# Kernel tuning notes

Hardware: AMD Instinct MI355X
Metric: run time of the kernel (lower is better)

The kernel has to match this reference:

```python
import jax, jax.numpy as jnp
import numpy as np

B, S, D = 4, 2048, 1024
H = 16
HD = D // H  # 64


def setup_inputs() -> dict:
    key = jax.random.key(0)
    ks = jax.random.split(key, 5)
    s = 0.02
    return {
        "x": jax.random.normal(ks[0], (B, S, D), dtype=jnp.float32),
        "w_qkv": jax.random.normal(ks[1], (D, 3 * D), dtype=jnp.float32) * s,
        "b_qkv": jnp.zeros((3 * D,), dtype=jnp.float32),
        "w_out": jax.random.normal(ks[2], (D, D), dtype=jnp.float32) * s,
        "b_out": jnp.zeros((D,), dtype=jnp.float32),
    }


def reference(x, w_qkv, b_qkv, w_out, b_out):
    b, s, d = x.shape
    qkv = x @ w_qkv + b_qkv                              # [b,s,3d]
    qkv = qkv.reshape(b, s, 3, H, HD)
    q = qkv[:, :, 0].transpose(0, 2, 1, 3)               # [b,h,s,hd]
    k = qkv[:, :, 1].transpose(0, 2, 1, 3)
    v = qkv[:, :, 2].transpose(0, 2, 1, 3)
    scale = 1.0 / jnp.sqrt(jnp.asarray(HD, dtype=x.dtype))
    scores = jnp.einsum("bhqd,bhkd->bhqk", q, k) * scale  # [b,h,s,s]
    causal = jnp.tril(jnp.ones((s, s), dtype=bool))
    scores = jnp.where(causal[None, None], scores, jnp.asarray(-jnp.inf, dtype=x.dtype))
    probs = jax.nn.softmax(scores, axis=-1)
    out = jnp.einsum("bhqk,bhkd->bhqd", probs, v)        # [b,h,s,hd]
    out = out.transpose(0, 2, 1, 3).reshape(b, s, d)
    return out @ w_out + b_out
```

## Files before the change

kernel.cpp:

```cpp
#include <hip/hip_runtime.h>
#include <hip/hip_bf16.h>

typedef __bf16 bf16_t;
typedef __bf16 bf16x4 __attribute__((ext_vector_type(4)));
typedef __bf16 bf16x8 __attribute__((ext_vector_type(8)));
typedef float f32x4 __attribute__((ext_vector_type(4)));

#define Bb 4
#define Ss 2048
#define Dd 1024
#define Hh 16
#define HDd 64

#define QSC 0.1803368801111244f

__device__ __forceinline__ void gld16(const bf16_t* g, bf16_t* l) {
  __builtin_amdgcn_global_load_lds(
      (const __attribute__((address_space(1))) unsigned int*)g,
      (__attribute__((address_space(3))) unsigned int*)l, 16, 0, 0);
}

__global__ __launch_bounds__(256) void prep(
    const float* __restrict__ x, bf16_t* __restrict__ Xc,
    const float* __restrict__ w_qkv, bf16_t* __restrict__ Wt1) {
  __shared__ bf16_t tile[32][33];
  const int b = blockIdx.x;
  const int tid = threadIdx.x;
  if (b < 8192) {
    int i = (b * 256 + tid) * 4;
    float4 v = *(const float4*)&x[i];
    bf16x4 o = {(bf16_t)v.x, (bf16_t)v.y, (bf16_t)v.z, (bf16_t)v.w};
    *(bf16x4*)&Xc[i] = o;
  } else {
    const int id = b - 8192;
    const int c0 = (id % 96) * 32, r0 = (id / 96) * 32;
    const int tx = tid & 31, ty = tid >> 5;
#pragma unroll
    for (int j = 0; j < 32; j += 8)
      tile[ty + j][tx] = (bf16_t)w_qkv[(size_t)(r0 + ty + j) * 3072 + c0 + tx];
    __syncthreads();
#pragma unroll
    for (int j = 0; j < 32; j += 8)
      Wt1[(size_t)(c0 + ty + j) * 1024 + r0 + tx] = tile[tx][ty + j];
  }
}

__global__ __launch_bounds__(256) void transpose_conv(
    const float* __restrict__ in, bf16_t* __restrict__ out, int R, int C) {
  __shared__ bf16_t tile[32][33];
  int c0 = blockIdx.x * 32, r0 = blockIdx.y * 32;
  int tx = threadIdx.x, ty = threadIdx.y;
#pragma unroll
  for (int j = 0; j < 32; j += 8)
    tile[ty + j][tx] = (bf16_t)in[(size_t)(r0 + ty + j) * C + c0 + tx];
  __syncthreads();
#pragma unroll
  for (int j = 0; j < 32; j += 8)
    out[(size_t)(c0 + ty + j) * R + r0 + tx] = tile[tx][ty + j];
}

template <int MODE>
__global__ __launch_bounds__(512, 2) void gemm_8p(
    const bf16_t* __restrict__ A, const bf16_t* __restrict__ Bt,
    const float* __restrict__ bias, float* __restrict__ outf,
    bf16_t* __restrict__ out0, bf16_t* __restrict__ out1,
    bf16_t* __restrict__ out2, int M, int N, int K) {
  const int tid = threadIdx.x;
  const int lane = tid & 63;
  const int wave = tid >> 6;
  const int quad = lane >> 4;
  const int lr = lane & 15;
  const int wr = wave >> 1;
  const int wc = wave & 1;
  const int m0 = blockIdx.y * 256;
  const int n0 = blockIdx.x * 128;

  __shared__ __align__(16) bf16_t As[3][256 * 64];
  __shared__ __align__(16) bf16_t Bs[3][128 * 64];

  const f32x4 zero = {0.f, 0.f, 0.f, 0.f};
  f32x4 acc[4][4];
#pragma unroll
  for (int mi = 0; mi < 4; ++mi)
#pragma unroll
    for (int ni = 0; ni < 4; ++ni) acc[mi][ni] = zero;

  int ar[4], ac[4], br[2], bc[2];
#pragma unroll
  for (int i = 0; i < 4; ++i) {
    int c = tid + i * 512;
    ar[i] = c >> 3;
    ac[i] = ((c & 7) ^ (ar[i] & 7)) * 8;
  }
#pragma unroll
  for (int i = 0; i < 2; ++i) {
    int c = tid + i * 512;
    br[i] = c >> 3;
    bc[i] = ((c & 7) ^ (br[i] & 7)) * 8;
  }

  const int nk = K >> 6;

  auto stageA = [&](int t, int s) {
    const int ko = t << 6;
#pragma unroll
    for (int i = 0; i < 4; ++i)
      gld16(&A[(size_t)(m0 + ar[i]) * K + ko + ac[i]],
            &As[s][(tid + i * 512) * 8]);
  };
  auto stageB = [&](int t, int s) {
    const int ko = t << 6;
#pragma unroll
    for (int i = 0; i < 2; ++i)
      gld16(&Bt[(size_t)(n0 + br[i]) * K + ko + bc[i]],
            &Bs[s][(tid + i * 512) * 8]);
  };

  stageA(0, 0); stageB(0, 0);
  stageA(1, 1); stageB(1, 1);
  asm volatile("s_waitcnt vmcnt(6)" ::: "memory");
  __builtin_amdgcn_s_barrier();

  const int sx = lr & 7;
  const int arow = wr * 64 + lr;
  const int brow = wc * 64 + lr;

  int scur = 0;
  for (int t = 0; t < nk; ++t) {
    const bf16_t* as = As[scur];
    const bf16_t* bs = Bs[scur];
    int s2 = scur + 2;
    if (s2 >= 3) s2 -= 3;
    const bool pre = (t + 2 < nk);
#pragma unroll
    for (int ks = 0; ks < 2; ++ks) {
      bf16x8 af[4], bfr[4];
      const int cx = (((ks << 2) | quad) ^ sx) * 8;
#pragma unroll
      for (int mi = 0; mi < 4; ++mi)
        af[mi] = *(const bf16x8*)&as[(arow + mi * 16) * 64 + cx];
#pragma unroll
      for (int ni = 0; ni < 4; ++ni)
        bfr[ni] = *(const bf16x8*)&bs[(brow + ni * 16) * 64 + cx];
      if (ks == 0) {
        if (pre) stageA(t + 2, s2);
      } else {
        if (pre) stageB(t + 2, s2);
      }
      __builtin_amdgcn_s_barrier();
      asm volatile("s_waitcnt lgkmcnt(0)" ::: "memory");
      __builtin_amdgcn_sched_barrier(0);
      __builtin_amdgcn_s_setprio(1);
#pragma unroll
      for (int mi = 0; mi < 4; ++mi)
#pragma unroll
        for (int ni = 0; ni < 4; ++ni)
          acc[mi][ni] = __builtin_amdgcn_mfma_f32_16x16x32_bf16(
              af[mi], bfr[ni], acc[mi][ni], 0, 0, 0);
      __builtin_amdgcn_s_setprio(0);
      if (ks == 0) {
        __builtin_amdgcn_s_barrier();
      } else if (t + 1 < nk) {
        if (pre)
          asm volatile("s_waitcnt vmcnt(6)" ::: "memory");
        else
          asm volatile("s_waitcnt vmcnt(0)" ::: "memory");
        __builtin_amdgcn_s_barrier();
      }
    }
    scur = (scur == 2) ? 0 : scur + 1;
  }

#pragma unroll
  for (int mi = 0; mi < 4; ++mi) {
    const int mbase = m0 + wr * 64 + mi * 16 + quad * 4;
#pragma unroll
    for (int ni = 0; ni < 4; ++ni) {
      const int n = n0 + wc * 64 + ni * 16 + lr;
      const float bv = bias[n];
      if (MODE == 1) {
#pragma unroll
        for (int r = 0; r < 4; ++r)
          outf[(size_t)(mbase + r) * N + n] = acc[mi][ni][r] + bv;
      } else {
        const int which = n >> 10;
        const int h = (n >> 6) & 15;
        const int hd = n & 63;
        const int b = mbase >> 11;
        const int s = mbase & 2047;
        if (which == 2) {
          bf16x4 pk = {(bf16_t)(acc[mi][ni][0] + bv),
                       (bf16_t)(acc[mi][ni][1] + bv),
                       (bf16_t)(acc[mi][ni][2] + bv),
                       (bf16_t)(acc[mi][ni][3] + bv)};
          *(bf16x4*)&out2[(((size_t)(b * Hh + h)) * HDd + hd) * Ss + s] = pk;
        } else {
          bf16_t* dst = (which == 0) ? out0 : out1;
          const float sc = (which == 0) ? QSC : 1.0f;
#pragma unroll
          for (int r = 0; r < 4; ++r)
            dst[(((size_t)(b * Hh + h)) * Ss + s + r) * HDd + hd] =
                (bf16_t)((acc[mi][ni][r] + bv) * sc);
        }
      }
    }
  }
}

__global__ __launch_bounds__(256) void attn_kernel(
    const bf16_t* __restrict__ Qg, const bf16_t* __restrict__ Kg,
    const bf16_t* __restrict__ Vtg, bf16_t* __restrict__ Og) {
  const int tid = threadIdx.x;
  const int lane = tid & 63;
  const int wave = tid >> 6;
  const int quad = lane >> 4;
  const int lr = lane & 15;
  const int l7 = lr & 7;

  const int bid = blockIdx.x;
  const int xcd = bid & 7;
  const int j = bid >> 3;
  const int bh = xcd * 8 + (j >> 3);
  const int p = j & 7;
  const int b = bh >> 4;
  const int h = bh & 15;
  const int wq = wave * 32;

  const bf16_t* Qp = Qg + (size_t)bh * Ss * HDd;
  const bf16_t* Kp = Kg + (size_t)bh * Ss * HDd;
  const bf16_t* Vp = Vtg + (size_t)bh * HDd * Ss;

  __shared__ bf16_t Ks[2][64 * 64];
  __shared__ bf16_t Vts[2][64 * 64];
  __shared__ bf16_t Ps[4][32 * 64];

  bf16x8 kreg[2], vreg[2];
  const int r0 = tid >> 3;
  const int c0 = (tid & 7) * 8;
  const int swz = ((tid & 7) ^ ((tid >> 3) & 7)) * 8;

  const f32x4 zero = {0.f, 0.f, 0.f, 0.f};
  bf16x8 ones1;
#pragma unroll
  for (int i = 0; i < 8; ++i) ones1[i] = (bf16_t)1.0f;

#pragma unroll
  for (int i = 0; i < 2; ++i) {
    kreg[i] = *(const bf16x8*)&Kp[(size_t)(r0 + i * 32) * HDd + c0];
    vreg[i] = *(const bf16x8*)&Vp[(size_t)(r0 + i * 32) * Ss + c0];
  }

  int cur = 0;
  for (int half = 0; half < 2; ++half) {
    const int qt = half ? p : 15 - p;
    const int qbase = qt * 128;
    const int ktiles = qt * 2 + 2;

    bf16x8 bq[2][2];
#pragma unroll
    for (int qt2 = 0; qt2 < 2; ++qt2)
#pragma unroll
      for (int kk2 = 0; kk2 < 2; ++kk2)
        bq[qt2][kk2] = *(const bf16x8*)&Qp[(size_t)(qbase + wq + qt2 * 16 +
                                                    lr) *
                                               HDd +
                                           kk2 * 32 + quad * 8];

    f32x4 oacc[4][2];
#pragma unroll
    for (int dt = 0; dt < 4; ++dt)
#pragma unroll
      for (int qt2 = 0; qt2 < 2; ++qt2) oacc[dt][qt2] = zero;
    f32x4 lacc[2];
    lacc[0] = zero;
    lacc[1] = zero;

    for (int kt = 0; kt < ktiles; ++kt) {
      const int kbase = kt * 64;

#pragma unroll
      for (int i = 0; i < 2; ++i) {
        *(bf16x8*)&Ks[cur][(r0 + i * 32) * 64 + swz] = kreg[i];
        *(bf16x8*)&Vts[cur][(r0 + i * 32) * 64 + swz] = vreg[i];
      }
      __syncthreads();

      const int nkb = (kt + 1 < ktiles) ? kbase + 64 : 0;
#pragma unroll
      for (int i = 0; i < 2; ++i) {
        kreg[i] = *(const bf16x8*)&Kp[(size_t)(nkb + r0 + i * 32) * HDd + c0];
        vreg[i] = *(const bf16x8*)&Vp[(size_t)(r0 + i * 32) * Ss + nkb + c0];
      }

      f32x4 sacc[4][2];
#pragma unroll
      for (int kt4 = 0; kt4 < 4; ++kt4)
#pragma unroll
        for (int qt2 = 0; qt2 < 2; ++qt2) sacc[kt4][qt2] = zero;
#pragma unroll
      for (int kk2 = 0; kk2 < 2; ++kk2) {
        const int rsl = (((kk2 << 2) | quad) ^ l7) * 8;
        bf16x8 ak[4];
#pragma unroll
        for (int kt4 = 0; kt4 < 4; ++kt4)
          ak[kt4] = *(const bf16x8*)&Ks[cur][(kt4 * 16 + lr) * 64 + rsl];
#pragma unroll
        for (int kt4 = 0; kt4 < 4; ++kt4)
#pragma unroll
          for (int qt2 = 0; qt2 < 2; ++qt2)
            sacc[kt4][qt2] = __builtin_amdgcn_mfma_f32_16x16x32_bf16(
                ak[kt4], bq[qt2][kk2], sacc[kt4][qt2], 0, 0, 0);
      }

      const bool edge = (kt >= 2 * qt);
#pragma unroll
      for (int kt4 = 0; kt4 < 4; ++kt4)
#pragma unroll
        for (int qt2 = 0; qt2 < 2; ++qt2)
#pragma unroll
          for (int r = 0; r < 4; ++r) {
            float s = sacc[kt4][qt2][r];
            if (edge) {
              const int qg = qbase + wq + qt2 * 16 + lr;
              const int kg = kbase + kt4 * 16 + quad * 4 + r;
              if (kg > qg) s = -1e30f;
            }
            sacc[kt4][qt2][r] = __builtin_amdgcn_exp2f(s);
          }

#pragma unroll
      for (int kt4 = 0; kt4 < 4; ++kt4) {
        const int psl = ((kt4 * 2 + (quad >> 1)) ^ l7) * 8 + (quad & 1) * 4;
#pragma unroll
        for (int qt2 = 0; qt2 < 2; ++qt2) {
          bf16x4 pk = {(bf16_t)sacc[kt4][qt2][0], (bf16_t)sacc[kt4][qt2][1],
                       (bf16_t)sacc[kt4][qt2][2], (bf16_t)sacc[kt4][qt2][3]};
          *(bf16x4*)&Ps[wave][(qt2 * 16 + lr) * 64 + psl] = pk;
        }
      }

#pragma unroll
      for (int kk2 = 0; kk2 < 2; ++kk2) {
        const int rsl = (((kk2 << 2) | quad) ^ l7) * 8;
        bf16x8 av[4], bp[2];
#pragma unroll
        for (int dt = 0; dt < 4; ++dt)
          av[dt] = *(const bf16x8*)&Vts[cur][(dt * 16 + lr) * 64 + rsl];
#pragma unroll
        for (int qt2 = 0; qt2 < 2; ++qt2)
          bp[qt2] = *(const bf16x8*)&Ps[wave][(qt2 * 16 + lr) * 64 + rsl];
#pragma unroll
        for (int dt = 0; dt < 4; ++dt)
#pragma unroll
          for (int qt2 = 0; qt2 < 2; ++qt2)
            oacc[dt][qt2] = __builtin_amdgcn_mfma_f32_16x16x32_bf16(
                av[dt], bp[qt2], oacc[dt][qt2], 0, 0, 0);
#pragma unroll
        for (int qt2 = 0; qt2 < 2; ++qt2)
          lacc[qt2] = __builtin_amdgcn_mfma_f32_16x16x32_bf16(
              ones1, bp[qt2], lacc[qt2], 0, 0, 0);
      }
      cur ^= 1;
    }

#pragma unroll
    for (int qt2 = 0; qt2 < 2; ++qt2) {
      const float inv = 1.f / lacc[qt2][0];
      const int qg = qbase + wq + qt2 * 16 + lr;
#pragma unroll
      for (int dt = 0; dt < 4; ++dt) {
        bf16x4 ov = {(bf16_t)(oacc[dt][qt2][0] * inv),
                     (bf16_t)(oacc[dt][qt2][1] * inv),
                     (bf16_t)(oacc[dt][qt2][2] * inv),
                     (bf16_t)(oacc[dt][qt2][3] * inv)};
        *(bf16x4*)&Og[((size_t)b * Ss + qg) * Dd + h * HDd + dt * 16 +
                      quad * 4] = ov;
      }
    }
  }
}

extern "C" void kernel_launch(void* const* d_in, const int* in_sizes, int n_in,
                              void* d_out, int out_size, void* d_ws,
                              size_t ws_size, hipStream_t stream) {
  const float* x = (const float*)d_in[0];
  const float* w_qkv = (const float*)d_in[1];
  const float* b_qkv = (const float*)d_in[2];
  const float* w_out = (const float*)d_in[3];
  const float* b_out = (const float*)d_in[4];
  float* out = (float*)d_out;

  bf16_t* Kb = (bf16_t*)d_ws;
  bf16_t* Vt = Kb + (size_t)Bb * Hh * Ss * HDd;
  bf16_t* slot3 = Vt + (size_t)Bb * Hh * Ss * HDd;
  bf16_t* Wt1 = slot3;
  bf16_t* Ob = slot3;
  bf16_t* Wt2 = Kb;
  bf16_t* Qb = (bf16_t*)d_out;
  bf16_t* Xc = (bf16_t*)d_out + (size_t)8192 * 1024;

  prep<<<11264, 256, 0, stream>>>(x, Xc, w_qkv, Wt1);

  gemm_8p<0><<<dim3(24, 32), 512, 0, stream>>>(
      Xc, Wt1, b_qkv, nullptr, Qb, Kb, Vt, 8192, 3072, 1024);

  attn_kernel<<<dim3(512), 256, 0, stream>>>(Qb, Kb, Vt, Ob);

  transpose_conv<<<dim3(32, 32), dim3(32, 8), 0, stream>>>(w_out, Wt2, 1024,
                                                           1024);

  gemm_8p<1><<<dim3(8, 32), 512, 0, stream>>>(
      Ob, Wt2, b_out, out, nullptr, nullptr, nullptr, 8192, 1024, 1024);
}
```

Before: 263.4 us.

## Use 256x256 tile GEMM for QKV projection and scalar row-sum in attention

Adds a gemm_wide kernel that computes the QKV projection with 256x256 output tiles, a K-step of 32 and a 4-stage LDS ring. Each wave now holds an 8x4 accumulator block, which raises arithmetic intensity and halves the number of blocks. In attention, the softmax denominator is no longer computed with extra MFMAs against a ones vector. Instead each lane accumulates its exp values in a float and a cross-lane shuffle reduction finishes the sum. The larger tile doubles accumulator register pressure with the 2-block occupancy hint, and the fp32 sum is taken before rounding to bf16, so it differs slightly from the bf16 P actually used in P·V.

```diff
diff --git a/kernel.cpp b/kernel.cpp
--- a/kernel.cpp
+++ b/kernel.cpp
@@ -60,7 +60,7 @@
 }
 
 template <int MODE>
-__global__ __launch_bounds__(512, 2) void gemm_8p(
+__global__ __launch_bounds__(512, 2) void gemm_wide(
     const bf16_t* __restrict__ A, const bf16_t* __restrict__ Bt,
     const float* __restrict__ bias, float* __restrict__ outf,
     bf16_t* __restrict__ out0, bf16_t* __restrict__ out1,
@@ -70,110 +70,107 @@
   const int wave = tid >> 6;
   const int quad = lane >> 4;
   const int lr = lane & 15;
-  const int wr = wave >> 1;
-  const int wc = wave & 1;
+  const int wr = wave >> 2;
+  const int wc = wave & 3;
   const int m0 = blockIdx.y * 256;
-  const int n0 = blockIdx.x * 128;
-
-  __shared__ __align__(16) bf16_t As[3][256 * 64];
-  __shared__ __align__(16) bf16_t Bs[3][128 * 64];
+  const int n0 = blockIdx.x * 256;
+
+  __shared__ __align__(16) bf16_t As[4][256 * 32];
+  __shared__ __align__(16) bf16_t Bs[4][256 * 32];
 
   const f32x4 zero = {0.f, 0.f, 0.f, 0.f};
-  f32x4 acc[4][4];
-#pragma unroll
-  for (int mi = 0; mi < 4; ++mi)
+  f32x4 acc[8][4];
+#pragma unroll
+  for (int mi = 0; mi < 8; ++mi)
 #pragma unroll
     for (int ni = 0; ni < 4; ++ni) acc[mi][ni] = zero;
 
-  int ar[4], ac[4], br[2], bc[2];
-#pragma unroll
-  for (int i = 0; i < 4; ++i) {
-    int c = tid + i * 512;
-    ar[i] = c >> 3;
-    ac[i] = ((c & 7) ^ (ar[i] & 7)) * 8;
-  }
+  int sr[2], sc[2];
 #pragma unroll
   for (int i = 0; i < 2; ++i) {
     int c = tid + i * 512;
-    br[i] = c >> 3;
-    bc[i] = ((c & 7) ^ (br[i] & 7)) * 8;
-  }
-
-  const int nk = K >> 6;
+    sr[i] = c >> 2;
+    sc[i] = ((c & 3) ^ ((sr[i] >> 1) & 3)) * 8;
+  }
+
+  const int nk = K >> 5;
 
   auto stageA = [&](int t, int s) {
-    const int ko = t << 6;
-#pragma unroll
-    for (int i = 0; i < 4; ++i)
-      gld16(&A[(size_t)(m0 + ar[i]) * K + ko + ac[i]],
+    const int ko = t << 5;
+#pragma unroll
+    for (int i = 0; i < 2; ++i)
+      gld16(&A[(size_t)(m0 + sr[i]) * K + ko + sc[i]],
             &As[s][(tid + i * 512) * 8]);
   };
   auto stageB = [&](int t, int s) {
-    const int ko = t << 6;
+    const int ko = t << 5;
 #pragma unroll
     for (int i = 0; i < 2; ++i)
-      gld16(&Bt[(size_t)(n0 + br[i]) * K + ko + bc[i]],
+      gld16(&Bt[(size_t)(n0 + sr[i]) * K + ko + sc[i]],
             &Bs[s][(tid + i * 512) * 8]);
   };
 
   stageA(0, 0); stageB(0, 0);
   stageA(1, 1); stageB(1, 1);
-  asm volatile("s_waitcnt vmcnt(6)" ::: "memory");
+  asm volatile("s_waitcnt vmcnt(4)" ::: "memory");
   __builtin_amdgcn_s_barrier();
 
-  const int sx = lr & 7;
-  const int arow = wr * 64 + lr;
-  const int brow = wc * 64 + lr;
-
-  int scur = 0;
+  const int cx = (quad ^ ((lr >> 1) & 3)) * 8;
+  const int abase = wr * 128 + lr;
+  const int bbase = wc * 64 + lr;
+
   for (int t = 0; t < nk; ++t) {
-    const bf16_t* as = As[scur];
-    const bf16_t* bs = Bs[scur];
-    int s2 = scur + 2;
-    if (s2 >= 3) s2 -= 3;
+    const bf16_t* as = As[t & 3];
+    const bf16_t* bs = Bs[t & 3];
+    const int s2 = (t + 2) & 3;
     const bool pre = (t + 2 < nk);
-#pragma unroll
-    for (int ks = 0; ks < 2; ++ks) {
-      bf16x8 af[4], bfr[4];
-      const int cx = (((ks << 2) | quad) ^ sx) * 8;
-#pragma unroll
-      for (int mi = 0; mi < 4; ++mi)
-        af[mi] = *(const bf16x8*)&as[(arow + mi * 16) * 64 + cx];
+    bf16x8 af[4], bfr[4];
+#pragma unroll
+    for (int ni = 0; ni < 4; ++ni)
+      bfr[ni] = *(const bf16x8*)&bs[(bbase + ni * 16) * 32 + cx];
+#pragma unroll
+    for (int mi = 0; mi < 4; ++mi)
+      af[mi] = *(const bf16x8*)&as[(abase + mi * 16) * 32 + cx];
+    if (pre) stageA(t + 2, s2);
+    __builtin_amdgcn_s_barrier();
+    asm volatile("s_waitcnt lgkmcnt(0)" ::: "memory");
+    __builtin_amdgcn_sched_barrier(0);
+    __builtin_amdgcn_s_setprio(1);
+#pragma unroll
+    for (int mi = 0; mi < 4; ++mi)
 #pragma unroll
       for (int ni = 0; ni < 4; ++ni)
-        bfr[ni] = *(const bf16x8*)&bs[(brow + ni * 16) * 64 + cx];
-      if (ks == 0) {
-        if (pre) stageA(t + 2, s2);
-      } else {
-        if (pre) stageB(t + 2, s2);
-      }
+        acc[mi][ni] = __builtin_amdgcn_mfma_f32_16x16x32_bf16(
+            af[mi], bfr[ni], acc[mi][ni], 0, 0, 0);
+    __builtin_amdgcn_s_setprio(0);
+    __builtin_amdgcn_s_barrier();
+#pragma unroll
+    for (int mi = 0; mi < 4; ++mi)
+      af[mi] = *(const bf16x8*)&as[(abase + (mi + 4) * 16) * 32 + cx];
+    if (pre) stageB(t + 2, s2);
+    __builtin_amdgcn_s_barrier();
+    asm volatile("s_waitcnt lgkmcnt(0)" ::: "memory");
+    __builtin_amdgcn_sched_barrier(0);
+    __builtin_amdgcn_s_setprio(1);
+#pragma unroll
+    for (int mi = 0; mi < 4; ++mi)
+#pragma unroll
+      for (int ni = 0; ni < 4; ++ni)
+        acc[mi + 4][ni] = __builtin_amdgcn_mfma_f32_16x16x32_bf16(
+            af[mi], bfr[ni], acc[mi + 4][ni], 0, 0, 0);
+    __builtin_amdgcn_s_setprio(0);
+    if (t + 1 < nk) {
+      if (pre)
+        asm volatile("s_waitcnt vmcnt(4)" ::: "memory");
+      else
+        asm volatile("s_waitcnt vmcnt(0)" ::: "memory");
       __builtin_amdgcn_s_barrier();
-      asm volatile("s_waitcnt lgkmcnt(0)" ::: "memory");
-      __builtin_amdgcn_sched_barrier(0);
-      __builtin_amdgcn_s_setprio(1);
-#pragma unroll
-      for (int mi = 0; mi < 4; ++mi)
-#pragma unroll
-        for (int ni = 0; ni < 4; ++ni)
-          acc[mi][ni] = __builtin_amdgcn_mfma_f32_16x16x32_bf16(
-              af[mi], bfr[ni], acc[mi][ni], 0, 0, 0);
-      __builtin_amdgcn_s_setprio(0);
-      if (ks == 0) {
-        __builtin_amdgcn_s_barrier();
-      } else if (t + 1 < nk) {
-        if (pre)
-          asm volatile("s_waitcnt vmcnt(6)" ::: "memory");
-        else
-          asm volatile("s_waitcnt vmcnt(0)" ::: "memory");
-        __builtin_amdgcn_s_barrier();
-      }
-    }
-    scur = (scur == 2) ? 0 : scur + 1;
-  }
-
-#pragma unroll
-  for (int mi = 0; mi < 4; ++mi) {
-    const int mbase = m0 + wr * 64 + mi * 16 + quad * 4;
+    }
+  }
+
+#pragma unroll
+  for (int mi = 0; mi < 8; ++mi) {
+    const int mbase = m0 + wr * 128 + mi * 16 + quad * 4;
 #pragma unroll
     for (int ni = 0; ni < 4; ++ni) {
       const int n = n0 + wc * 64 + ni * 16 + lr;
@@ -196,11 +193,159 @@
           *(bf16x4*)&out2[(((size_t)(b * Hh + h)) * HDd + hd) * Ss + s] = pk;
         } else {
           bf16_t* dst = (which == 0) ? out0 : out1;
-          const float sc = (which == 0) ? QSC : 1.0f;
+          const float sc2 = (which == 0) ? QSC : 1.0f;
 #pragma unroll
           for (int r = 0; r < 4; ++r)
             dst[(((size_t)(b * Hh + h)) * Ss + s + r) * HDd + hd] =
-                (bf16_t)((acc[mi][ni][r] + bv) * sc);
+                (bf16_t)((acc[mi][ni][r] + bv) * sc2);
+        }
+      }
+    }
+  }
+}
+
+template <int MODE>
+__global__ __launch_bounds__(512, 2) void gemm_8p(
+    const bf16_t* __restrict__ A, const bf16_t* __restrict__ Bt,
+    const float* __restrict__ bias, float* __restrict__ outf,
+    bf16_t* __restrict__ out0, bf16_t* __restrict__ out1,
+    bf16_t* __restrict__ out2, int M, int N, int K) {
+  const int tid = threadIdx.x;
+  const int lane = tid & 63;
+  const int wave = tid >> 6;
+  const int quad = lane >> 4;
+  const int lr = lane & 15;
+  const int wr = wave >> 1;
+  const int wc = wave & 1;
+  const int m0 = blockIdx.y * 256;
+  const int n0 = blockIdx.x * 128;
+
+  __shared__ __align__(16) bf16_t As[3][256 * 64];
+  __shared__ __align__(16) bf16_t Bs[3][128 * 64];
+
+  const f32x4 zero = {0.f, 0.f, 0.f, 0.f};
+  f32x4 acc[4][4];
+#pragma unroll
+  for (int mi = 0; mi < 4; ++mi)
+#pragma unroll
+    for (int ni = 0; ni < 4; ++ni) acc[mi][ni] = zero;
+
+  int ar[4], ac[4], br[2], bc[2];
+#pragma unroll
+  for (int i = 0; i < 4; ++i) {
+    int c = tid + i * 512;
+    ar[i] = c >> 3;
+    ac[i] = ((c & 7) ^ (ar[i] & 7)) * 8;
+  }
+#pragma unroll
+  for (int i = 0; i < 2; ++i) {
+    int c = tid + i * 512;
+    br[i] = c >> 3;
+    bc[i] = ((c & 7) ^ (br[i] & 7)) * 8;
+  }
+
+  const int nk = K >> 6;
+
+  auto stageA = [&](int t, int s) {
+    const int ko = t << 6;
+#pragma unroll
+    for (int i = 0; i < 4; ++i)
+      gld16(&A[(size_t)(m0 + ar[i]) * K + ko + ac[i]],
+            &As[s][(tid + i * 512) * 8]);
+  };
+  auto stageB = [&](int t, int s) {
+    const int ko = t << 6;
+#pragma unroll
+    for (int i = 0; i < 2; ++i)
+      gld16(&Bt[(size_t)(n0 + br[i]) * K + ko + bc[i]],
+            &Bs[s][(tid + i * 512) * 8]);
+  };
+
+  stageA(0, 0); stageB(0, 0);
+  stageA(1, 1); stageB(1, 1);
+  asm volatile("s_waitcnt vmcnt(6)" ::: "memory");
+  __builtin_amdgcn_s_barrier();
+
+  const int sx = lr & 7;
+  const int arow = wr * 64 + lr;
+  const int brow = wc * 64 + lr;
+
+  int scur = 0;
+  for (int t = 0; t < nk; ++t) {
+    const bf16_t* as = As[scur];
+    const bf16_t* bs = Bs[scur];
+    int s2 = scur + 2;
+    if (s2 >= 3) s2 -= 3;
+    const bool pre = (t + 2 < nk);
+#pragma unroll
+    for (int ks = 0; ks < 2; ++ks) {
+      bf16x8 af[4], bfr[4];
+      const int cx = (((ks << 2) | quad) ^ sx) * 8;
+#pragma unroll
+      for (int mi = 0; mi < 4; ++mi)
+        af[mi] = *(const bf16x8*)&as[(arow + mi * 16) * 64 + cx];
+#pragma unroll
+      for (int ni = 0; ni < 4; ++ni)
+        bfr[ni] = *(const bf16x8*)&bs[(brow + ni * 16) * 64 + cx];
+      if (ks == 0) {
+        if (pre) stageA(t + 2, s2);
+      } else {
+        if (pre) stageB(t + 2, s2);
+      }
+      __builtin_amdgcn_s_barrier();
+      asm volatile("s_waitcnt lgkmcnt(0)" ::: "memory");
+      __builtin_amdgcn_sched_barrier(0);
+      __builtin_amdgcn_s_setprio(1);
+#pragma unroll
+      for (int mi = 0; mi < 4; ++mi)
+#pragma unroll
+        for (int ni = 0; ni < 4; ++ni)
+          acc[mi][ni] = __builtin_amdgcn_mfma_f32_16x16x32_bf16(
+              af[mi], bfr[ni], acc[mi][ni], 0, 0, 0);
+      __builtin_amdgcn_s_setprio(0);
+      if (ks == 0) {
+        __builtin_amdgcn_s_barrier();
+      } else if (t + 1 < nk) {
+        if (pre)
+          asm volatile("s_waitcnt vmcnt(6)" ::: "memory");
+        else
+          asm volatile("s_waitcnt vmcnt(0)" ::: "memory");
+        __builtin_amdgcn_s_barrier();
+      }
+    }
+    scur = (scur == 2) ? 0 : scur + 1;
+  }
+
+#pragma unroll
+  for (int mi = 0; mi < 4; ++mi) {
+    const int mbase = m0 + wr * 64 + mi * 16 + quad * 4;
+#pragma unroll
+    for (int ni = 0; ni < 4; ++ni) {
+      const int n = n0 + wc * 64 + ni * 16 + lr;
+      const float bv = bias[n];
+      if (MODE == 1) {
+#pragma unroll
+        for (int r = 0; r < 4; ++r)
+          outf[(size_t)(mbase + r) * N + n] = acc[mi][ni][r] + bv;
+      } else {
+        const int which = n >> 10;
+        const int h = (n >> 6) & 15;
+        const int hd = n & 63;
+        const int b = mbase >> 11;
+        const int s = mbase & 2047;
+        if (which == 2) {
+          bf16x4 pk = {(bf16_t)(acc[mi][ni][0] + bv),
+                       (bf16_t)(acc[mi][ni][1] + bv),
+                       (bf16_t)(acc[mi][ni][2] + bv),
+                       (bf16_t)(acc[mi][ni][3] + bv)};
+          *(bf16x4*)&out2[(((size_t)(b * Hh + h)) * HDd + hd) * Ss + s] = pk;
+        } else {
+          bf16_t* dst = (which == 0) ? out0 : out1;
+          const float sc2 = (which == 0) ? QSC : 1.0f;
+#pragma unroll
+          for (int r = 0; r < 4; ++r)
+            dst[(((size_t)(b * Hh + h)) * Ss + s + r) * HDd + hd] =
+                (bf16_t)((acc[mi][ni][r] + bv) * sc2);
         }
       }
     }
@@ -240,9 +385,6 @@
   const int swz = ((tid & 7) ^ ((tid >> 3) & 7)) * 8;
 
   const f32x4 zero = {0.f, 0.f, 0.f, 0.f};
-  bf16x8 ones1;
-#pragma unroll
-  for (int i = 0; i < 8; ++i) ones1[i] = (bf16_t)1.0f;
 
 #pragma unroll
   for (int i = 0; i < 2; ++i) {
@@ -271,9 +413,7 @@
     for (int dt = 0; dt < 4; ++dt)
 #pragma unroll
       for (int qt2 = 0; qt2 < 2; ++qt2) oacc[dt][qt2] = zero;
-    f32x4 lacc[2];
-    lacc[0] = zero;
-    lacc[1] = zero;
+    float l_run[2] = {0.f, 0.f};
 
     for (int kt = 0; kt < ktiles; ++kt) {
       const int kbase = kt * 64;
@@ -325,7 +465,9 @@
               const int kg = kbase + kt4 * 16 + quad * 4 + r;
               if (kg > qg) s = -1e30f;
             }
-            sacc[kt4][qt2][r] = __builtin_amdgcn_exp2f(s);
+            const float pv = __builtin_amdgcn_exp2f(s);
+            sacc[kt4][qt2][r] = pv;
+            l_run[qt2] += pv;
           }
 
 #pragma unroll
@@ -355,17 +497,19 @@
           for (int qt2 = 0; qt2 < 2; ++qt2)
             oacc[dt][qt2] = __builtin_amdgcn_mfma_f32_16x16x32_bf16(
                 av[dt], bp[qt2], oacc[dt][qt2], 0, 0, 0);
-#pragma unroll
-        for (int qt2 = 0; qt2 < 2; ++qt2)
-          lacc[qt2] = __builtin_amdgcn_mfma_f32_16x16x32_bf16(
-              ones1, bp[qt2], lacc[qt2], 0, 0, 0);
       }
       cur ^= 1;
     }
 
 #pragma unroll
     for (int qt2 = 0; qt2 < 2; ++qt2) {
-      const float inv = 1.f / lacc[qt2][0];
+      l_run[qt2] += __shfl_xor(l_run[qt2], 16, 64);
+      l_run[qt2] += __shfl_xor(l_run[qt2], 32, 64);
+    }
+
+#pragma unroll
+    for (int qt2 = 0; qt2 < 2; ++qt2) {
+      const float inv = 1.f / l_run[qt2];
       const int qg = qbase + wq + qt2 * 16 + lr;
 #pragma unroll
       for (int dt = 0; dt < 4; ++dt) {
@@ -401,7 +545,7 @@
 
   prep<<<11264, 256, 0, stream>>>(x, Xc, w_qkv, Wt1);
 
-  gemm_8p<0><<<dim3(24, 32), 512, 0, stream>>>(
+  gemm_wide<0><<<dim3(12, 32), 512, 0, stream>>>(
       Xc, Wt1, b_qkv, nullptr, Qb, Kb, Vt, 8192, 3072, 1024);
 
   attn_kernel<<<dim3(512), 256, 0, stream>>>(Qb, Kb, Vt, Ob);
```

Measured after the change: 264.5 us. About the same (+0.4%).
